# Performance work log

Hardware: AMD Instinct MI355X
Metric: run time of the kernel (lower is better)

Reference implementation:

```python
import math
import jax, jax.numpy as jnp
import numpy as np

B, L, ENC_IN, D_MODEL, D_FF, E_LAYERS, N_HEADS, FACTOR = 4, 2048, 32, 512, 2048, 2, 8, 5


def layer_norm(x, g, b, eps=1e-5):
    mu = jnp.mean(x, axis=-1, keepdims=True)
    var = jnp.mean((x - mu) ** 2, axis=-1, keepdims=True)
    return (x - mu) / jnp.sqrt(var + eps) * g + b


def positional_encoding(length, d_model):
    pos = np.arange(length, dtype=np.float32)[:, None]
    div = np.exp(np.arange(0, d_model, 2, dtype=np.float32) * -(math.log(10000.0) / d_model))
    pe = np.zeros((length, d_model), dtype=np.float32)
    pe[:, 0::2] = np.sin(pos * div)
    pe[:, 1::2] = np.cos(pos * div)
    return jnp.asarray(pe)


def circ_conv1d(x, w, b=None):
    # x: [B,L,Cin], w: [Cout,Cin,3]; kernel 3, circular padding 1, stride 1 -> [B,L,Cout]
    xc = jnp.transpose(x, (0, 2, 1))
    xc = jnp.pad(xc, ((0, 0), (0, 0), (1, 1)), mode='wrap')
    y = jax.lax.conv_general_dilated(xc, w, (1,), 'VALID',
                                     dimension_numbers=('NCH', 'OIH', 'NCH'))
    if b is not None:
        y = y + b[None, :, None]
    return jnp.transpose(y, (0, 2, 1))


def prob_attention(Q, K, V, key):
    # Q,K,V: [B,H,L,D]; ProbAttention(mask_flag=False, factor=5)
    Bq, H, Lq, D = Q.shape
    sample_k = min(FACTOR * int(math.ceil(math.log(Lq))), Lq)  # U_part
    n_top = min(FACTOR * int(math.ceil(math.log(Lq))), Lq)    # u
    idx = jax.random.randint(key, (Lq, sample_k), 0, Lq)
    K_samp = K[:, :, idx, :]                                  # [B,H,L,sample_k,D]
    QK_samp = jnp.einsum('bhld,bhlud->bhlu', Q, K_samp)
    M = QK_samp.max(axis=-1) - QK_samp.sum(axis=-1) / Lq      # sparsity measure [B,H,L]
    _, M_top = jax.lax.top_k(M, n_top)                        # [B,H,u]
    Q_red = jnp.take_along_axis(Q, M_top[..., None], axis=2)  # [B,H,u,D]
    scores = jnp.einsum('bhud,bhkd->bhuk', Q_red, K) / math.sqrt(D)
    attn = jax.nn.softmax(scores, axis=-1)
    upd = jnp.einsum('bhuk,bhkd->bhud', attn, V)
    # initial context = mean of V (mask_flag=False), overwritten at top-u rows
    ctx = jnp.broadcast_to(jnp.mean(V, axis=2, keepdims=True), (Bq, H, Lq, D))
    bi = jnp.arange(Bq)[:, None, None]
    hi = jnp.arange(H)[None, :, None]
    return ctx.at[bi, hi, M_top].set(upd)


def attention_layer(x, Wq, bq, Wk, bk, Wv, bv, Wo, bo, key):
    Bx, Lx, dm = x.shape
    D = dm // N_HEADS
    def split(h):
        return h.reshape(Bx, Lx, N_HEADS, D).transpose(0, 2, 1, 3)
    q = split(x @ Wq.T + bq)
    k = split(x @ Wk.T + bk)
    v = split(x @ Wv.T + bv)
    ctx = prob_attention(q, k, v, key)
    ctx = ctx.transpose(0, 2, 1, 3).reshape(Bx, Lx, dm)
    return ctx @ Wo.T + bo


def encoder_layer(x, Wq, bq, Wk, bk, Wv, bv, Wo, bo, W1, b1, W2, b2, g1, be1, g2, be2, key):
    x = x + attention_layer(x, Wq, bq, Wk, bk, Wv, bv, Wo, bo, key)
    x = layer_norm(x, g1, be1)
    y = jax.nn.gelu(x @ W1.T + b1, approximate=False)  # conv1 (kernel 1) + gelu
    y = y @ W2.T + b2                                  # conv2 (kernel 1)
    return layer_norm(x + y, g2, be2)


def conv_distil(x, w, b, bn_g, bn_b):
    y = circ_conv1d(x, w, b)
    mu = jnp.mean(y, axis=(0, 1))                      # BatchNorm1d (training-mode stats)
    var = jnp.mean((y - mu) ** 2, axis=(0, 1))
    y = (y - mu) / jnp.sqrt(var + 1e-5) * bn_g + bn_b
    y = jax.nn.elu(y)
    yt = jnp.transpose(y, (0, 2, 1))                   # MaxPool1d(k=3, s=2, p=1)
    yt = jax.lax.reduce_window(yt, -jnp.inf, jax.lax.max,
                               (1, 1, 3), (1, 1, 2), [(0, 0), (0, 0), (1, 1)])
    return jnp.transpose(yt, (0, 2, 1))


def setup_inputs() -> dict:
    key = jax.random.key(0)
    ks = iter(jax.random.split(key, 32))
    def nrm(shape, sc=0.02):
        return jax.random.normal(next(ks), shape, jnp.float32) * sc
    return {
        'x_enc': jax.random.normal(next(ks), (B, L, ENC_IN), jnp.float32),
        'tok_w': nrm((D_MODEL, ENC_IN, 3), 0.1),
        'Wq': nrm((E_LAYERS, D_MODEL, D_MODEL)), 'bq': jnp.zeros((E_LAYERS, D_MODEL)),
        'Wk': nrm((E_LAYERS, D_MODEL, D_MODEL)), 'bk': jnp.zeros((E_LAYERS, D_MODEL)),
        'Wv': nrm((E_LAYERS, D_MODEL, D_MODEL)), 'bv': jnp.zeros((E_LAYERS, D_MODEL)),
        'Wo': nrm((E_LAYERS, D_MODEL, D_MODEL)), 'bo': jnp.zeros((E_LAYERS, D_MODEL)),
        'W1': nrm((E_LAYERS, D_FF, D_MODEL)), 'b1': jnp.zeros((E_LAYERS, D_FF)),
        'W2': nrm((E_LAYERS, D_MODEL, D_FF)), 'b2': jnp.zeros((E_LAYERS, D_MODEL)),
        'ln1_g': jnp.ones((E_LAYERS, D_MODEL)), 'ln1_b': jnp.zeros((E_LAYERS, D_MODEL)),
        'ln2_g': jnp.ones((E_LAYERS, D_MODEL)), 'ln2_b': jnp.zeros((E_LAYERS, D_MODEL)),
        'conv_w': nrm((D_MODEL, D_MODEL, 3)), 'conv_b': jnp.zeros((D_MODEL,)),
        'bn_g': jnp.ones((D_MODEL,)), 'bn_b': jnp.zeros((D_MODEL,)),
        'normf_g': jnp.ones((D_MODEL,)), 'normf_b': jnp.zeros((D_MODEL,)),
        'proj_w': nrm((ENC_IN, D_MODEL)), 'proj_b': jnp.zeros((ENC_IN,)),
    }


def reference(x_enc, tok_w, Wq, bq, Wk, bk, Wv, bv, Wo, bo, W1, b1, W2, b2,
              ln1_g, ln1_b, ln2_g, ln2_b, conv_w, conv_b, bn_g, bn_b,
              normf_g, normf_b, proj_w, proj_b):
    keys = jax.random.split(jax.random.key(42), E_LAYERS)
    # DataEmbedding: circular token conv (no bias) + sinusoidal positional embedding
    x = circ_conv1d(x_enc, tok_w) + positional_encoding(x_enc.shape[1], D_MODEL)[None]
    for i in range(E_LAYERS):
        x = encoder_layer(x, Wq[i], bq[i], Wk[i], bk[i], Wv[i], bv[i], Wo[i], bo[i],
                          W1[i], b1[i], W2[i], b2[i],
                          ln1_g[i], ln1_b[i], ln2_g[i], ln2_b[i], keys[i])
        if i == 0:  # single distillation ConvLayer after first encoder layer
            x = conv_distil(x, conv_w, conv_b, bn_g, bn_b)
    x = layer_norm(x, normf_g, normf_b)
    out = x @ proj_w.T + proj_b
    return out[:, :L]  # [:, :seq_len] slice (no-op after distillation halves length)
```

## Files before the change

kernel.cpp:

```cpp
#include <hip/hip_runtime.h>
#include <cstdint>
#include <cmath>


#define NB 4
#define DM 512
#define NH 8
#define HD 64
#define QS 1536

typedef unsigned short ushort_t;
typedef __bf16 bf16x8 __attribute__((ext_vector_type(8)));
typedef float floatx4 __attribute__((ext_vector_type(4)));
typedef unsigned short ushort8_t __attribute__((ext_vector_type(8)));

__device__ inline ushort_t f2b(float f) {
  uint32_t u = __float_as_uint(f);
  uint32_t r = (u + 0x7fffu + ((u >> 16) & 1u)) >> 16;
  return (ushort_t)r;
}
__device__ inline float b2f(ushort_t u) {
  return __uint_as_float((uint32_t)u << 16);
}

__global__ void castqkv_k(const float* __restrict__ Wq,
                          const float* __restrict__ Wk,
                          const float* __restrict__ Wv,
                          ushort_t* __restrict__ out) {
  int gid = blockIdx.x * 256 + threadIdx.x;
  if (gid >= 393216) return;
  int ly = gid / 196608, r4 = gid - ly * 196608;
  int r = r4 >> 7, c4 = r4 & 127;
  int sel = r >> 9, srow = r & 511;
  const float* src = (sel == 0 ? Wq : sel == 1 ? Wk : Wv) + ly * 262144 +
                     srow * 512 + c4 * 4;
  float4 v = *(const float4*)src;
  ushort4 o;
  o.x = f2b(v.x); o.y = f2b(v.y); o.z = f2b(v.z); o.w = f2b(v.w);
  ((ushort4*)out)[ly * 196608 + r * 128 + c4] = o;
}

__global__ void castw3_k(const float* __restrict__ Wo,
                         const float* __restrict__ W1,
                         const float* __restrict__ W2,
                         const float* __restrict__ tw,
                         ushort_t* __restrict__ oWo, ushort_t* __restrict__ oW1,
                         ushort_t* __restrict__ oW2, ushort_t* __restrict__ otw) {
  int gid = blockIdx.x * 256 + threadIdx.x;
  if (gid >= 1191936) return;
  const float* src;
  ushort4* dst;
  int i;
  if (gid < 131072) { src = Wo; dst = (ushort4*)oWo; i = gid; }
  else if (gid < 655360) { src = W1; dst = (ushort4*)oW1; i = gid - 131072; }
  else if (gid < 1179648) { src = W2; dst = (ushort4*)oW2; i = gid - 655360; }
  else { src = tw; dst = (ushort4*)otw; i = gid - 1179648; }
  float4 v = ((const float4*)src)[i];
  ushort4 o;
  o.x = f2b(v.x); o.y = f2b(v.y); o.z = f2b(v.z); o.w = f2b(v.w);
  dst[i] = o;
}

__global__ void castw_conv_k(const float* __restrict__ in,
                             ushort_t* __restrict__ out) {
  int gid = blockIdx.x * 256 + threadIdx.x;
  int d = gid / 1536, r = gid - d * 1536;
  int t = r >> 9, i = r & 511;
  out[gid] = f2b(in[d * 1536 + i * 3 + t]);
}

__global__ void castproj_k(const float* __restrict__ w,
                           float* __restrict__ wt) {
  int gid = blockIdx.x * 256 + threadIdx.x;
  int k = gid >> 5, n = gid & 31;
  wt[gid] = w[n * 512 + k];
}

__global__ void setup_small_k(const float* __restrict__ bq,
                              const float* __restrict__ bk,
                              const float* __restrict__ bv,
                              float* __restrict__ ZB,
                              float* __restrict__ BQKV) {
  int gid = blockIdx.x * 256 + threadIdx.x;
  if (gid >= 3584) return;
  if (gid < 512) { ZB[gid] = 0.f; return; }
  int g = gid - 512;
  int layer = g / 1536, r = g - layer * 1536;
  float v;
  if (r < 512) v = bq[layer * 512 + r];
  else if (r < 1024) v = bk[layer * 512 + r - 512];
  else v = bv[layer * 512 + r - 1024];
  BQKV[g] = v;
}

__host__ __device__ inline void threefry2x32(uint32_t k0, uint32_t k1,
                                             uint32_t c0, uint32_t c1,
                                             uint32_t* o0, uint32_t* o1) {
  uint32_t ks0 = k0, ks1 = k1, ks2 = k0 ^ k1 ^ 0x1BD11BDAu;
  uint32_t x0 = c0 + ks0;
  uint32_t x1 = c1 + ks1;
  const uint32_t rotA[4] = {13u, 15u, 26u, 6u};
  const uint32_t rotB[4] = {17u, 29u, 16u, 24u};
  uint32_t ks[3] = {ks0, ks1, ks2};
  #pragma unroll
  for (int i = 0; i < 5; ++i) {
    const uint32_t* r = (i & 1) ? rotB : rotA;
    #pragma unroll
    for (int j = 0; j < 4; ++j) {
      x0 += x1;
      x1 = (x1 << r[j]) | (x1 >> (32u - r[j]));
      x1 ^= x0;
    }
    x0 += ks[(i + 1) % 3];
    x1 += ks[(i + 2) % 3] + (uint32_t)(i + 1);
  }
  *o0 = x0; *o1 = x1;
}

__global__ void gen_idx_k(int* __restrict__ idx, int n, int mask,
                          uint32_t k0, uint32_t k1) {
  int i = blockIdx.x * 256 + threadIdx.x;
  if (i < n) {
    uint32_t o0, o1;
    threefry2x32(k0, k1, 0u, (uint32_t)i, &o0, &o1);
    idx[i] = (int)((o0 ^ o1) & (uint32_t)mask);
  }
}

__device__ inline float wave_sum64(float v) {
  #pragma unroll
  for (int o = 32; o > 0; o >>= 1) v += __shfl_xor(v, o, 64);
  return v;
}

__global__ void pe_k(float* __restrict__ pe) {
  int i = blockIdx.x * 256 + threadIdx.x;
  int d = i & 511, l = i >> 9;
  int j2 = d & ~1;
  float div = expf((float)j2 * -1.7988946039e-2f);
  float ang = (float)l * div;
  pe[i] = (d & 1) ? cosf(ang) : sinf(ang);
}

__global__ void im2col_tok_k(const float* __restrict__ xe,
                             ushort_t* __restrict__ A) {
  int gid = blockIdx.x * 256 + threadIdx.x;
  int col = gid % 96;
  int row = gid / 96;
  int c = col / 3, t = col - c * 3;
  int b = row >> 11, l = row & 2047;
  int ls = (l + t - 1) & 2047;
  A[gid] = f2b(xe[((size_t)b * 2048 + ls) * 32 + c]);
}

__device__ inline void gload16(const ushort_t* g, ushort_t* l) {
  __builtin_amdgcn_global_load_lds(
      (const __attribute__((address_space(1))) unsigned int*)(const void*)g,
      (__attribute__((address_space(3))) unsigned int*)(void*)l, 16, 0, 0);
}

template <int TM, int CONV, int GELU, int OMODE, int ADDPE, int SPLITK>
__global__ __launch_bounds__(512, 4) void mgemm_k(
    const ushort_t* __restrict__ A, const ushort_t* __restrict__ W,
    const float* __restrict__ bias, float* __restrict__ Cf,
    float* __restrict__ Cf2, ushort_t* __restrict__ Cb,
    const float* __restrict__ pe, int X, int ldc, int K) {
  constexpr int MT = TM / 64;
  constexpr int AG = TM / 128;
  constexpr int BUFSZ = (TM + 128) * 32;
  constexpr int SHSZ = (2 * BUFSZ > 18432) ? 2 * BUFSZ : 18432;
  __shared__ __align__(16) ushort_t SH[SHSZ];
  int id = blockIdx.x;
  int half = 0;
  if (SPLITK == 2) {
    int nb = gridDim.x >> 1;
    if (id >= nb) { half = 1; id -= nb; }
  }
  int kbase = half * (K >> 1);
  int KK = (SPLITK == 2) ? (K >> 1) : K;
  int cc = id & 7, j = id >> 3;
  int bx = j % X;
  int by = (j / X) * 8 + cc;
  int m0 = by * TM, n0 = bx * 128;
  int t = threadIdx.x;
  int lane = t & 63, wv = t >> 6;
  int rl = lane >> 2, cl = (lane & 3) * 8;
  int RaA = wv * (16 * AG);
  int RaB = wv * 16;
  const ushort_t* gA[AG];
  int cbv[AG], clrv[AG], lAoff[AG];
  #pragma unroll
  for (int g = 0; g < AG; ++g) {
    int ar = m0 + RaA + g * 16 + rl;
    gA[g] = A + (size_t)ar * K + kbase + cl;
    cbv[g] = ar >> 11;
    clrv[g] = ar & 2047;
    lAoff[g] = (RaA + g * 16) * 32;
  }
  const ushort_t* gB = W + (size_t)(n0 + RaB + rl) * K + kbase + cl;
  int lBoff = TM * 32 + RaB * 32;

  int quad = lane >> 4, lr = lane & 15;
  int wm = wv >> 1, wn = wv & 1;

  floatx4 acc[MT][4] = {};
  #pragma unroll
  for (int g = 0; g < AG; ++g) {
    if (CONV) {
      int kg = kbase;
      int tt = kg >> 9;
      int c = (kg & 511) + cl;
      int ls = (clrv[g] + tt - 1) & 2047;
      gload16(A + ((size_t)(cbv[g] * 2048 + ls) * 512 + c), SH + lAoff[g]);
    } else {
      gload16(gA[g], SH + lAoff[g]);
    }
  }
  gload16(gB, SH + lBoff);
  __syncthreads();
  int cur = 0;
  for (int ks = 0; ks < KK; ks += 32) {
    int nxt = ks + 32;
    if (nxt < KK) {
      int bb = (cur ^ 1) * BUFSZ;
      #pragma unroll
      for (int g = 0; g < AG; ++g) {
        if (CONV) {
          int kg = kbase + nxt;
          int tt = kg >> 9;
          int c = (kg & 511) + cl;
          int ls = (clrv[g] + tt - 1) & 2047;
          gload16(A + ((size_t)(cbv[g] * 2048 + ls) * 512 + c),
                  SH + bb + lAoff[g]);
        } else {
          gload16(gA[g] + nxt, SH + bb + lAoff[g]);
        }
      }
      gload16(gB + nxt, SH + bb + lBoff);
    }
    const ushort_t* Ab = SH + cur * BUFSZ;
    const ushort_t* Bb = Ab + TM * 32;
    bf16x8 av[MT], bv[4];
    #pragma unroll
    for (int mt = 0; mt < MT; ++mt)
      av[mt] =
          *(const bf16x8*)&Ab[(wm * (16 * MT) + mt * 16 + lr) * 32 + quad * 8];
    #pragma unroll
    for (int nt = 0; nt < 4; ++nt)
      bv[nt] = *(const bf16x8*)&Bb[(wn * 64 + nt * 16 + lr) * 32 + quad * 8];
    #pragma unroll
    for (int mt = 0; mt < MT; ++mt)
      #pragma unroll
      for (int nt = 0; nt < 4; ++nt)
        acc[mt][nt] = __builtin_amdgcn_mfma_f32_16x16x32_bf16(
            av[mt], bv[nt], acc[mt][nt], 0, 0, 0);
    __syncthreads();
    cur ^= 1;
  }

  if (SPLITK == 2) {
    float* dst = half ? Cf2 : Cf;
    #pragma unroll
    for (int nt = 0; nt < 4; ++nt) {
      int col = n0 + wn * 64 + nt * 16 + lr;
      #pragma unroll
      for (int mt = 0; mt < MT; ++mt) {
        int row0 = m0 + wm * (16 * MT) + mt * 16 + quad * 4;
        #pragma unroll
        for (int r = 0; r < 4; ++r)
          dst[(size_t)(row0 + r) * ldc + col] = acc[mt][nt][r];
      }
    }
  } else if (OMODE == 0) {
    #pragma unroll
    for (int nt = 0; nt < 4; ++nt) {
      int col = n0 + wn * 64 + nt * 16 + lr;
      float bsv = bias[col];
      #pragma unroll
      for (int mt = 0; mt < MT; ++mt) {
        int row0 = m0 + wm * (16 * MT) + mt * 16 + quad * 4;
        #pragma unroll
        for (int r = 0; r < 4; ++r) {
          int row = row0 + r;
          float v = acc[mt][nt][r] + bsv;
          if (ADDPE) v += pe[(size_t)(row & 2047) * ldc + col];
          if (GELU) v = 0.5f * v * (1.0f + erff(v * 0.70710678118654752f));
          Cf[(size_t)row * ldc + col] = v;
        }
      }
    }
  } else {
    ushort_t* ep = SH + wv * 2304;
    #pragma unroll
    for (int p = 0; p < MT / 2; ++p) {
      #pragma unroll
      for (int nt = 0; nt < 4; ++nt) {
        int col = n0 + wn * 64 + nt * 16 + lr;
        float bsv = bias[col];
        #pragma unroll
        for (int ml = 0; ml < 2; ++ml) {
          int mt = p * 2 + ml;
          #pragma unroll
          for (int r = 0; r < 4; ++r) {
            int row = m0 + wm * (16 * MT) + mt * 16 + quad * 4 + r;
            float v = acc[mt][nt][r] + bsv;
            if (ADDPE) v += pe[(size_t)(row & 2047) * ldc + col];
            if (GELU) v = 0.5f * v * (1.0f + erff(v * 0.70710678118654752f));
            if (OMODE == 2) Cf[(size_t)row * ldc + col] = v;
            ep[(ml * 16 + quad * 4 + r) * 72 + nt * 16 + lr] = f2b(v);
          }
        }
      }
      int r8 = lane >> 3, c8 = (lane & 7) * 8;
      #pragma unroll
      for (int i = 0; i < 4; ++i) {
        int row = i * 8 + r8;
        ushort8_t vv = *(const ushort8_t*)&ep[row * 72 + c8];
        *(ushort8_t*)&Cb[(size_t)(m0 + wm * (16 * MT) + p * 32 + row) * ldc +
                         n0 + wn * 64 + c8] = vv;
      }
    }
  }
}

__global__ __launch_bounds__(256) void proj_k(
    const float* __restrict__ A, const float* __restrict__ Wt,
    const float* __restrict__ bias, float* __restrict__ C) {
  int t = threadIdx.x;
  int n = t & 31, ml = t >> 5;
  int m = blockIdx.x * 8 + ml;
  const float* a = A + (size_t)m * DM;
  float a0 = 0.f, a1 = 0.f, a2 = 0.f, a3 = 0.f;
  #pragma unroll 4
  for (int k = 0; k < DM; k += 4) {
    float4 av = *(const float4*)&a[k];
    a0 += av.x * Wt[k * 32 + n];
    a1 += av.y * Wt[(k + 1) * 32 + n];
    a2 += av.z * Wt[(k + 2) * 32 + n];
    a3 += av.w * Wt[(k + 3) * 32 + n];
  }
  C[(size_t)m * 32 + n] = (a0 + a2) + (a1 + a3) + bias[n];
}

__global__ __launch_bounds__(128) void ln_k(
    const float* __restrict__ A, const float* __restrict__ Bres,
    const float* __restrict__ Bres2, const float* __restrict__ cbias,
    const float* __restrict__ g, const float* __restrict__ be,
    float* __restrict__ O, ushort_t* __restrict__ Ob) {
  int r = blockIdx.x, t = threadIdx.x;
  __shared__ float lds[2];
  float4 v = ((const float4*)(A + (size_t)r * DM))[t];
  if (Bres) {
    float4 u = ((const float4*)(Bres + (size_t)r * DM))[t];
    v.x += u.x; v.y += u.y; v.z += u.z; v.w += u.w;
  }
  if (Bres2) {
    float4 u = ((const float4*)(Bres2 + (size_t)r * DM))[t];
    v.x += u.x; v.y += u.y; v.z += u.z; v.w += u.w;
  }
  if (cbias) {
    float4 u = ((const float4*)cbias)[t];
    v.x += u.x; v.y += u.y; v.z += u.z; v.w += u.w;
  }
  float s = wave_sum64(v.x + v.y + v.z + v.w);
  int w = t >> 6;
  if ((t & 63) == 0) lds[w] = s;
  __syncthreads();
  float mu = (lds[0] + lds[1]) * (1.0f / 512.0f);
  __syncthreads();
  float dx = v.x - mu, dy = v.y - mu, dz = v.z - mu, dw = v.w - mu;
  float sq = wave_sum64(dx * dx + dy * dy + dz * dz + dw * dw);
  if ((t & 63) == 0) lds[w] = sq;
  __syncthreads();
  float var = (lds[0] + lds[1]) * (1.0f / 512.0f);
  float inv = 1.0f / sqrtf(var + 1e-5f);
  float4 gv = ((const float4*)g)[t];
  float4 bv = ((const float4*)be)[t];
  float4 o;
  o.x = dx * inv * gv.x + bv.x;
  o.y = dy * inv * gv.y + bv.y;
  o.z = dz * inv * gv.z + bv.z;
  o.w = dw * inv * gv.w + bv.w;
  ((float4*)(O + (size_t)r * DM))[t] = o;
  if (Ob) {
    ushort4 ob;
    ob.x = f2b(o.x); ob.y = f2b(o.y); ob.z = f2b(o.z); ob.w = f2b(o.w);
    ((ushort4*)(Ob + (size_t)r * DM))[t] = ob;
  }
}

template <int UU>
__global__ __launch_bounds__(256) void qk_m_k(
    const ushort_t* __restrict__ QKVb, const int* __restrict__ idx,
    float* __restrict__ Mout, int Lx) {
  int l = blockIdx.x;
  int b = threadIdx.x >> 6;
  int lane = threadIdx.x & 63;
  const ushort_t* qp = QKVb + ((size_t)b * Lx + l) * QS + lane * 8;
  float q[8];
  {
    ushort8_t qv = *(const ushort8_t*)qp;
    #pragma unroll
    for (int c = 0; c < 8; ++c) q[c] = b2f(qv[c]);
  }
  const ushort_t* Kbase = QKVb + (size_t)b * Lx * QS + 512 + lane * 8;
  const int* ip = idx + (size_t)l * UU;
  float maxv = -INFINITY, sumv = 0.f;
  #pragma unroll
  for (int u0 = 0; u0 < UU; u0 += 8) {
    ushort8_t kv[8];
    #pragma unroll
    for (int j = 0; j < 8; ++j) {
      if (u0 + j < UU)
        kv[j] = *(const ushort8_t*)(Kbase + (size_t)ip[u0 + j] * QS);
    }
    #pragma unroll
    for (int j = 0; j < 8; ++j) {
      if (u0 + j < UU) {
        float p = 0.f;
        #pragma unroll
        for (int c = 0; c < 8; ++c) p += q[c] * b2f(kv[j][c]);
        p += __shfl_xor(p, 1, 64);
        p += __shfl_xor(p, 2, 64);
        p += __shfl_xor(p, 4, 64);
        maxv = fmaxf(maxv, p);
        sumv += p;
      }
    }
  }
  if ((lane & 7) == 0) {
    int h = lane >> 3;
    Mout[(size_t)(b * 8 + h) * Lx + l] = maxv - sumv / (float)Lx;
  }
}

__global__ __launch_bounds__(1024) void topk_k(
    const float* __restrict__ Mbuf, int* __restrict__ Mtop, int Lx, int U) {
  int nch = Lx >> 8;
  int bh = blockIdx.x / nch, ch = blockIdx.x % nch;
  const float* m = Mbuf + (size_t)bh * Lx;
  __shared__ float sm[2048];
  __shared__ int part[1024];
  int t = threadIdx.x;
  int c = t & 255, q = t >> 8;
  for (int i = t; i < Lx; i += 1024) sm[i] = m[i];
  __syncthreads();
  int i0 = (ch << 8) + c;
  float v0 = sm[i0];
  int r0 = 0;
  int qlen = Lx >> 2;
  int j0 = q * qlen, j1 = j0 + qlen;
  for (int j = j0; j < j1; j += 4) {
    float4 mj = *(const float4*)&sm[j];
    r0 += (mj.x > v0) || (mj.x == v0 && (j + 0) < i0);
    r0 += (mj.y > v0) || (mj.y == v0 && (j + 1) < i0);
    r0 += (mj.z > v0) || (mj.z == v0 && (j + 2) < i0);
    r0 += (mj.w > v0) || (mj.w == v0 && (j + 3) < i0);
  }
  part[t] = r0;
  __syncthreads();
  if (q == 0) {
    int r = part[c] + part[c + 256] + part[c + 512] + part[c + 768];
    if (r < U) Mtop[bh * U + r] = i0;
  }
}

__global__ __launch_bounds__(512) void meanv1_k(const ushort_t* __restrict__ QKVb,
                                                float* __restrict__ part,
                                                int Lx) {
  int b = blockIdx.x >> 4, chunk = blockIdx.x & 15;
  int rows = Lx >> 4;
  int t = threadIdx.x;
  const ushort_t* vp =
      QKVb + ((size_t)b * Lx + (size_t)chunk * rows) * QS + 1024 + t;
  float s = 0.f;
  for (int l = 0; l < rows; ++l) s += b2f(vp[(size_t)l * QS]);
  part[(size_t)blockIdx.x * DM + t] = s;
}
__global__ __launch_bounds__(512) void meanv2_k(const float* __restrict__ part,
                                                float* __restrict__ mv,
                                                int Lx) {
  int b = blockIdx.x, t = threadIdx.x;
  float s = 0.f;
  #pragma unroll
  for (int c = 0; c < 16; ++c) s += part[(size_t)(b * 16 + c) * DM + t];
  mv[b * DM + t] = s / (float)Lx;
}

__global__ void fillctx_k(ushort_t* __restrict__ ctx,
                          const float* __restrict__ mv, int Lx) {
  size_t i4 = (size_t)blockIdx.x * 256 + threadIdx.x;
  int col4 = (int)(i4 & 127);
  size_t row = i4 >> 7;
  int b = (int)(row / (size_t)Lx);
  const float* m = mv + b * DM + col4 * 4;
  ushort4 o;
  o.x = f2b(m[0]); o.y = f2b(m[1]); o.z = f2b(m[2]); o.w = f2b(m[3]);
  ((ushort4*)ctx)[i4] = o;
}

template <int UP>
__global__ __launch_bounds__(256) void attn_mfma_k(
    const ushort_t* __restrict__ QKVb, const int* __restrict__ Mtop,
    float* __restrict__ part, int Lx, int U, int nblk) {
  __shared__ ushort_t Ps[4][UP * 72];
  __shared__ ushort_t Vs[4][64 * 64];
  int bh = blockIdx.x / nblk, blkc = blockIdx.x % nblk;
  int h = bh & 7, b = bh >> 3;
  int t = threadIdx.x;
  int wv = t >> 6, lane = t & 63;
  int quad = lane >> 4, lr = lane & 15;
  int chunk = blkc * 4 + wv;
  int k0 = chunk * 64;
  const ushort_t* Qb = QKVb + (size_t)b * Lx * QS + h * HD;
  const ushort_t* Kb = Qb + 512;
  const ushort_t* Vb = Qb + 1024;

  bf16x8 qf[3][2];
  #pragma unroll
  for (int mt = 0; mt < 3; ++mt) {
    int u = mt * 16 + lr;
    int qi = Mtop[bh * U + (u < U ? u : U - 1)];
    const ushort_t* qp = Qb + (size_t)qi * QS + quad * 8;
    qf[mt][0] = *(const bf16x8*)qp;
    qf[mt][1] = *(const bf16x8*)(qp + 32);
  }

  ushort_t* vs = Vs[wv];
  #pragma unroll
  for (int i = 0; i < 8; ++i) {
    int cid = i * 64 + lane;
    int k = cid >> 3, c = cid & 7;
    ushort8_t v = *(const ushort8_t*)(Vb + (size_t)(k0 + k) * QS + c * 8);
    *(ushort8_t*)&vs[k * 64 + ((c * 8) ^ (((k >> 3) & 3) << 4))] = v;
  }

  floatx4 Sa[3][4] = {};
  #pragma unroll
  for (int kt = 0; kt < 4; ++kt) {
    const ushort_t* kp = Kb + (size_t)(k0 + kt * 16 + lr) * QS + quad * 8;
    bf16x8 kf0 = *(const bf16x8*)kp;
    bf16x8 kf1 = *(const bf16x8*)(kp + 32);
    #pragma unroll
    for (int mt = 0; mt < 3; ++mt) {
      Sa[mt][kt] = __builtin_amdgcn_mfma_f32_16x16x32_bf16(
          qf[mt][0], kf0, Sa[mt][kt], 0, 0, 0);
      Sa[mt][kt] = __builtin_amdgcn_mfma_f32_16x16x32_bf16(
          qf[mt][1], kf1, Sa[mt][kt], 0, 0, 0);
    }
  }

  float m_[3][4], l_[3][4];
  #pragma unroll
  for (int mt = 0; mt < 3; ++mt) {
    #pragma unroll
    for (int kt = 0; kt < 4; ++kt) Sa[mt][kt] *= 0.125f;
    #pragma unroll
    for (int r = 0; r < 4; ++r) {
      float mx = fmaxf(fmaxf(Sa[mt][0][r], Sa[mt][1][r]),
                       fmaxf(Sa[mt][2][r], Sa[mt][3][r]));
      #pragma unroll
      for (int o = 1; o <= 8; o <<= 1) mx = fmaxf(mx, __shfl_xor(mx, o, 64));
      float rs = 0.f;
      #pragma unroll
      for (int kt = 0; kt < 4; ++kt) {
        float e = __expf(Sa[mt][kt][r] - mx);
        Sa[mt][kt][r] = e;
        rs += e;
      }
      #pragma unroll
      for (int o = 1; o <= 8; o <<= 1) rs += __shfl_xor(rs, o, 64);
      m_[mt][r] = mx;
      l_[mt][r] = rs;
    }
  }

  ushort_t* ps = Ps[wv];
  floatx4 Oa[3][4] = {};
  #pragma unroll
  for (int pass = 0; pass < 2; ++pass) {
    #pragma unroll
    for (int mt = 0; mt < 3; ++mt)
      #pragma unroll
      for (int kt = 0; kt < 4; ++kt)
        #pragma unroll
        for (int r = 0; r < 4; ++r) {
          float e = Sa[mt][kt][r];
          ushort_t hb = f2b(e);
          ps[(mt * 16 + quad * 4 + r) * 72 + kt * 16 + lr] = hb;
          Sa[mt][kt][r] = e - b2f(hb);
        }
    #pragma unroll
    for (int kk = 0; kk < 2; ++kk) {
      bf16x8 pf[3];
      #pragma unroll
      for (int mt = 0; mt < 3; ++mt)
        pf[mt] = *(const bf16x8*)&ps[(mt * 16 + lr) * 72 + kk * 32 + quad * 8];
      #pragma unroll
      for (int nt = 0; nt < 4; ++nt) {
        ushort8_t vt;
        #pragma unroll
        for (int j = 0; j < 8; ++j)
          vt[j] = vs[(kk * 32 + quad * 8 + j) * 64 +
                     ((nt * 16 + lr) ^ (quad << 4))];
        bf16x8 vf = *(bf16x8*)&vt;
        #pragma unroll
        for (int mt = 0; mt < 3; ++mt)
          Oa[mt][nt] = __builtin_amdgcn_mfma_f32_16x16x32_bf16(
              pf[mt], vf, Oa[mt][nt], 0, 0, 0);
      }
    }
  }

  float* pb = part + (size_t)(bh * (nblk * 4) + chunk) * U * 66;
  #pragma unroll
  for (int mt = 0; mt < 3; ++mt) {
    #pragma unroll
    for (int r = 0; r < 4; ++r) {
      int u = mt * 16 + quad * 4 + r;
      if (u < U) {
        #pragma unroll
        for (int nt = 0; nt < 4; ++nt)
          pb[(size_t)u * 66 + nt * 16 + lr] = Oa[mt][nt][r];
        if (lr == 0) {
          pb[(size_t)u * 66 + 64] = m_[mt][r];
          pb[(size_t)u * 66 + 65] = l_[mt][r];
        }
      }
    }
  }
}

__global__ __launch_bounds__(64) void attn_merge_k(
    const float* __restrict__ part, const int* __restrict__ Mtop,
    ushort_t* __restrict__ ctx, int Lx, int U, int nchunk) {
  int bu = blockIdx.x;
  int u = bu % U, bh = bu / U;
  int h = bh & 7, b = bh >> 3;
  int d = threadIdx.x;
  float M = -INFINITY;
  for (int c = 0; c < nchunk; ++c)
    M = fmaxf(M, part[((size_t)(bh * nchunk + c) * U + u) * 66 + 64]);
  float L = 0.f, O = 0.f;
  for (int c = 0; c < nchunk; ++c) {
    const float* pp = part + ((size_t)(bh * nchunk + c) * U + u) * 66;
    float w = __expf(pp[64] - M);
    L += pp[65] * w;
    O += pp[d] * w;
  }
  int qi = Mtop[bh * U + u];
  ctx[((size_t)b * Lx + qi) * DM + h * HD + d] = f2b(O / L);
}

__global__ __launch_bounds__(256) void bn1_k(const float* __restrict__ Y0,
                                             const float* __restrict__ Y1,
                                             const float* __restrict__ cb,
                                             float* __restrict__ ps,
                                             float* __restrict__ pq) {
  int blk = blockIdx.x;
  int t = threadIdx.x;
  float cb0 = cb[t], cb1 = cb[t + 256];
  float s0 = 0, q0 = 0, s1 = 0, q1 = 0;
  const float* b0 = Y0 + (size_t)blk * 256 * DM;
  const float* b1 = Y1 + (size_t)blk * 256 * DM;
  for (int r = 0; r < 256; ++r) {
    float a = b0[(size_t)r * DM + t] + b1[(size_t)r * DM + t] + cb0;
    float b = b0[(size_t)r * DM + t + 256] + b1[(size_t)r * DM + t + 256] + cb1;
    s0 += a; q0 += a * a; s1 += b; q1 += b * b;
  }
  ps[blk * DM + t] = s0; ps[blk * DM + t + 256] = s1;
  pq[blk * DM + t] = q0; pq[blk * DM + t + 256] = q1;
}
__global__ __launch_bounds__(512) void bn2_k(const float* __restrict__ ps,
                                             const float* __restrict__ pq,
                                             float* __restrict__ mu,
                                             float* __restrict__ var) {
  int t = threadIdx.x;
  float s = 0, q = 0;
  #pragma unroll
  for (int c = 0; c < 32; ++c) { s += ps[c * DM + t]; q += pq[c * DM + t]; }
  float m = s * (1.0f / 8192.f);
  mu[t] = m;
  var[t] = q * (1.0f / 8192.f) - m * m;
}

__global__ void bnpool_k(const float* __restrict__ Y0,
                         const float* __restrict__ Y1,
                         const float* __restrict__ cb,
                         const float* __restrict__ mu,
                         const float* __restrict__ var,
                         const float* __restrict__ g,
                         const float* __restrict__ be, float* __restrict__ O,
                         ushort_t* __restrict__ Ob) {
  size_t i = (size_t)blockIdx.x * 256 + threadIdx.x;
  int c = (int)(i & 511);
  size_t row = i >> 9;
  int lo = (int)(row & 1023);
  int b = (int)(row >> 10);
  float sc = g[c] / sqrtf(var[c] + 1e-5f);
  float sh = be[c] - mu[c] * sc;
  float cbv = cb[c];
  int l0 = 2 * lo - 1;
  float m = -INFINITY;
  #pragma unroll
  for (int tt = 0; tt < 3; ++tt) {
    int l = l0 + tt;
    if (l >= 0 && l < 2048) {
      size_t off = ((size_t)b * 2048 + l) * DM + c;
      float v = (Y0[off] + Y1[off] + cbv) * sc + sh;
      v = v > 0.f ? v : expm1f(v);
      m = fmaxf(m, v);
    }
  }
  O[i] = m;
  Ob[i] = f2b(m);
}

extern "C" void kernel_launch(void* const* d_in, const int* in_sizes, int n_in,
                              void* d_out, int out_size, void* d_ws,
                              size_t ws_size, hipStream_t stream) {
  (void)in_sizes; (void)n_in; (void)out_size; (void)ws_size;
  const float* x_enc  = (const float*)d_in[0];
  const float* tok_w  = (const float*)d_in[1];
  const float* Wq     = (const float*)d_in[2];
  const float* bq     = (const float*)d_in[3];
  const float* Wk     = (const float*)d_in[4];
  const float* bk     = (const float*)d_in[5];
  const float* Wv     = (const float*)d_in[6];
  const float* bv     = (const float*)d_in[7];
  const float* Wo     = (const float*)d_in[8];
  const float* bo     = (const float*)d_in[9];
  const float* W1     = (const float*)d_in[10];
  const float* b1     = (const float*)d_in[11];
  const float* W2     = (const float*)d_in[12];
  const float* b2     = (const float*)d_in[13];
  const float* ln1_g  = (const float*)d_in[14];
  const float* ln1_b  = (const float*)d_in[15];
  const float* ln2_g  = (const float*)d_in[16];
  const float* ln2_b  = (const float*)d_in[17];
  const float* conv_w = (const float*)d_in[18];
  const float* conv_b = (const float*)d_in[19];
  const float* bn_g   = (const float*)d_in[20];
  const float* bn_b   = (const float*)d_in[21];
  const float* normf_g = (const float*)d_in[22];
  const float* normf_b = (const float*)d_in[23];
  const float* proj_w = (const float*)d_in[24];
  const float* proj_b = (const float*)d_in[25];
  float* out = (float*)d_out;
  float* ws = (float*)d_ws;

  float* X    = ws;
  float* Y2B  = ws + 4194304;
  float* SCR  = ws + 8388608;
  ushort_t* CTXb = (ushort_t*)(ws + 16777216);
  float* Y2   = ws + 20971520;
  float* Mb   = ws + 25165824;
  float* MV   = ws + 25231360;
  float* MVP  = ws + 25233408;
  float* BNps = ws + 25266176;
  float* BNpq = ws + 25282560;
  float* BNmu = ws + 25298944;
  float* BNvr = ws + 25299456;
  float* ZB   = ws + 25299968;
  float* BQKV = ws + 25300480;
  int*   IDX  = (int*)(ws + 25303552);
  int*   MT   = (int*)(ws + 25385472);
  ushort_t* U0   = (ushort_t*)(ws + 25386752);
  ushort_t* Xb   = U0;
  ushort_t* Hb   = U0 + 4194304;
  ushort_t* QKVb = Hb;
  ushort_t* Wqkvb= U0 + 20971520;
  ushort_t* Wob  = U0 + 22544384;
  ushort_t* W1b  = U0 + 23068672;
  ushort_t* W2b  = U0 + 25165824;
  ushort_t* Cwb  = U0 + 27262976;
  ushort_t* Twb  = U0 + 28049408;
  ushort_t* Atok = U0 + 28098560;
  float* PEf = ws + 39829248;
  float* PWt = ws + 40877824;

  castqkv_k<<<1536, 256, 0, stream>>>(Wq, Wk, Wv, Wqkvb);
  castw3_k<<<4656, 256, 0, stream>>>(Wo, W1, W2, tok_w, Wob, W1b, W2b, Twb);
  castw_conv_k<<<3072, 256, 0, stream>>>(conv_w, Cwb);
  castproj_k<<<64, 256, 0, stream>>>(proj_w, PWt);
  setup_small_k<<<14, 256, 0, stream>>>(bq, bk, bv, ZB, BQKV);
  pe_k<<<4096, 256, 0, stream>>>(PEf);
  im2col_tok_k<<<3072, 256, 0, stream>>>(x_enc, Atok);

  mgemm_k<128, 0, 0, 2, 1, 1><<<256, 512, 0, stream>>>(
      Atok, Twb, ZB, X, nullptr, Xb, PEf, 4, DM, 96);

  for (int layer = 0; layer < 2; ++layer) {
    const int Lx = (layer == 0) ? 2048 : 1024;
    const int U  = (layer == 0) ? 40 : 35;
    const int M  = NB * Lx;
    const int Yt = M / 128;
    const int NCHT = Lx / 64;
    const int NBLK = NCHT / 4;

    uint32_t kl0, kl1, s0, s1;
    threefry2x32(0u, 42u, 0u, (uint32_t)layer, &kl0, &kl1);
    threefry2x32(kl0, kl1, 0u, 1u, &s0, &s1);
    int nidx = Lx * U;
    gen_idx_k<<<(nidx + 255) / 256, 256, 0, stream>>>(IDX, nidx, Lx - 1, s0, s1);

    mgemm_k<128, 0, 0, 1, 0, 1><<<12 * Yt, 512, 0, stream>>>(
        Xb, Wqkvb + (size_t)layer * 786432, BQKV + layer * 1536, nullptr,
        nullptr, QKVb, nullptr, 12, QS, DM);

    if (layer == 0)
      qk_m_k<40><<<Lx, 256, 0, stream>>>(QKVb, IDX, Mb, Lx);
    else
      qk_m_k<35><<<Lx, 256, 0, stream>>>(QKVb, IDX, Mb, Lx);
    topk_k<<<NB * NH * (Lx >> 8), 1024, 0, stream>>>(Mb, MT, Lx, U);
    meanv1_k<<<NB * 16, 512, 0, stream>>>(QKVb, MVP, Lx);
    meanv2_k<<<NB, 512, 0, stream>>>(MVP, MV, Lx);
    fillctx_k<<<(M * DM / 4) / 256, 256, 0, stream>>>(CTXb, MV, Lx);
    attn_mfma_k<48><<<NB * NH * NBLK, 256, 0, stream>>>(QKVb, MT, Y2, Lx, U,
                                                        NBLK);
    attn_merge_k<<<NB * NH * U, 64, 0, stream>>>(Y2, MT, CTXb, Lx, U, NCHT);

    mgemm_k<128, 0, 0, 0, 0, 2><<<2 * 4 * Yt, 512, 0, stream>>>(
        CTXb, Wob + (size_t)layer * 262144, nullptr, Y2, Y2B, nullptr,
        nullptr, 4, DM, DM);
    ln_k<<<M, 128, 0, stream>>>(X, Y2, Y2B, bo + layer * DM,
                                ln1_g + layer * DM, ln1_b + layer * DM, X, Xb);

    mgemm_k<128, 0, 1, 1, 0, 1><<<16 * Yt, 512, 0, stream>>>(
        Xb, W1b + (size_t)layer * 1048576, b1 + layer * 2048, nullptr, nullptr,
        Hb, nullptr, 16, 2048, DM);
    mgemm_k<128, 0, 0, 0, 0, 2><<<2 * 4 * Yt, 512, 0, stream>>>(
        Hb, W2b + (size_t)layer * 1048576, nullptr, Y2, Y2B, nullptr,
        nullptr, 4, DM, 2048);
    ln_k<<<M, 128, 0, stream>>>(X, Y2, Y2B, b2 + layer * DM,
                                ln2_g + layer * DM, ln2_b + layer * DM, X, Xb);

    if (layer == 0) {
      mgemm_k<128, 1, 0, 0, 0, 2><<<2 * 4 * 64, 512, 0, stream>>>(
          Xb, Cwb, nullptr, Y2, Y2B, nullptr, nullptr, 4, DM, 1536);
      bn1_k<<<32, 256, 0, stream>>>(Y2, Y2B, conv_b, BNps, BNpq);
      bn2_k<<<1, 512, 0, stream>>>(BNps, BNpq, BNmu, BNvr);
      bnpool_k<<<(NB * 1024 * 512) / 256, 256, 0, stream>>>(
          Y2, Y2B, conv_b, BNmu, BNvr, bn_g, bn_b, X, Xb);
    }
  }

  ln_k<<<NB * 1024, 128, 0, stream>>>(X, nullptr, nullptr, nullptr, normf_g,
                                      normf_b, SCR, nullptr);
  proj_k<<<512, 256, 0, stream>>>(SCR, PWt, proj_b, out);
}
```

Measured before the change: 618.3 us.

## Triple-buffer GEMM LDS pipeline with explicit vmcnt waits and single barrier

```diff
diff --git a/kernel.cpp b/kernel.cpp
--- a/kernel.cpp
+++ b/kernel.cpp
@@ -168,7 +168,7 @@
   constexpr int MT = TM / 64;
   constexpr int AG = TM / 128;
   constexpr int BUFSZ = (TM + 128) * 32;
-  constexpr int SHSZ = (2 * BUFSZ > 18432) ? 2 * BUFSZ : 18432;
+  constexpr int SHSZ = (3 * BUFSZ > 18432) ? 3 * BUFSZ : 18432;
   __shared__ __align__(16) ushort_t SH[SHSZ];
   int id = blockIdx.x;
   int half = 0;
@@ -203,40 +203,46 @@
   int quad = lane >> 4, lr = lane & 15;
   int wm = wv >> 1, wn = wv & 1;
 
+  auto STAGE = [&](int kst, int buf) {
+    int bb = buf * BUFSZ;
+    int ko = kst << 5;
+    #pragma unroll
+    for (int g = 0; g < AG; ++g) {
+      if (CONV) {
+        int kg = kbase + ko;
+        int tt = kg >> 9;
+        int c = (kg & 511) + cl;
+        int ls = (clrv[g] + tt - 1) & 2047;
+        gload16(A + ((size_t)(cbv[g] * 2048 + ls) * 512 + c),
+                SH + bb + lAoff[g]);
+      } else {
+        gload16(gA[g] + ko, SH + bb + lAoff[g]);
+      }
+    }
+    gload16(gB + ko, SH + bb + lBoff);
+  };
+
   floatx4 acc[MT][4] = {};
-  #pragma unroll
-  for (int g = 0; g < AG; ++g) {
-    if (CONV) {
-      int kg = kbase;
-      int tt = kg >> 9;
-      int c = (kg & 511) + cl;
-      int ls = (clrv[g] + tt - 1) & 2047;
-      gload16(A + ((size_t)(cbv[g] * 2048 + ls) * 512 + c), SH + lAoff[g]);
+  int nt = KK >> 5;
+  STAGE(0, 0);
+  if (nt > 1) STAGE(1, 1);
+  int cur = 0;
+  for (int it = 0; it < nt; ++it) {
+    if (it < nt - 1) {
+      if constexpr (AG == 1)
+        asm volatile("s_waitcnt vmcnt(2)" ::: "memory");
+      else
+        asm volatile("s_waitcnt vmcnt(3)" ::: "memory");
     } else {
-      gload16(gA[g], SH + lAoff[g]);
-    }
-  }
-  gload16(gB, SH + lBoff);
-  __syncthreads();
-  int cur = 0;
-  for (int ks = 0; ks < KK; ks += 32) {
-    int nxt = ks + 32;
-    if (nxt < KK) {
-      int bb = (cur ^ 1) * BUFSZ;
-      #pragma unroll
-      for (int g = 0; g < AG; ++g) {
-        if (CONV) {
-          int kg = kbase + nxt;
-          int tt = kg >> 9;
-          int c = (kg & 511) + cl;
-          int ls = (clrv[g] + tt - 1) & 2047;
-          gload16(A + ((size_t)(cbv[g] * 2048 + ls) * 512 + c),
-                  SH + bb + lAoff[g]);
-        } else {
-          gload16(gA[g] + nxt, SH + bb + lAoff[g]);
-        }
-      }
-      gload16(gB + nxt, SH + bb + lBoff);
+      asm volatile("s_waitcnt vmcnt(0)" ::: "memory");
+    }
+    __builtin_amdgcn_s_barrier();
+    __builtin_amdgcn_sched_barrier(0);
+    int nx = it + 2;
+    if (nx < nt) {
+      int nb3 = cur + 2;
+      if (nb3 >= 3) nb3 -= 3;
+      STAGE(nx, nb3);
     }
     const ushort_t* Ab = SH + cur * BUFSZ;
     const ushort_t* Bb = Ab + TM * 32;
@@ -246,35 +252,37 @@
       av[mt] =
           *(const bf16x8*)&Ab[(wm * (16 * MT) + mt * 16 + lr) * 32 + quad * 8];
     #pragma unroll
-    for (int nt = 0; nt < 4; ++nt)
-      bv[nt] = *(const bf16x8*)&Bb[(wn * 64 + nt * 16 + lr) * 32 + quad * 8];
+    for (int nt2 = 0; nt2 < 4; ++nt2)
+      bv[nt2] = *(const bf16x8*)&Bb[(wn * 64 + nt2 * 16 + lr) * 32 + quad * 8];
     #pragma unroll
     for (int mt = 0; mt < MT; ++mt)
       #pragma unroll
-      for (int nt = 0; nt < 4; ++nt)
-        acc[mt][nt] = __builtin_amdgcn_mfma_f32_16x16x32_bf16(
-            av[mt], bv[nt], acc[mt][nt], 0, 0, 0);
-    __syncthreads();
-    cur ^= 1;
-  }
+      for (int nt2 = 0; nt2 < 4; ++nt2)
+        acc[mt][nt2] = __builtin_amdgcn_mfma_f32_16x16x32_bf16(
+            av[mt], bv[nt2], acc[mt][nt2], 0, 0, 0);
+    asm volatile("s_waitcnt lgkmcnt(0)" ::: "memory");
+    __builtin_amdgcn_sched_barrier(0);
+    cur = (cur == 2) ? 0 : cur + 1;
+  }
+  __syncthreads();
 
   if (SPLITK == 2) {
     float* dst = half ? Cf2 : Cf;
     #pragma unroll
-    for (int nt = 0; nt < 4; ++nt) {
-      int col = n0 + wn * 64 + nt * 16 + lr;
+    for (int nt2 = 0; nt2 < 4; ++nt2) {
+      int col = n0 + wn * 64 + nt2 * 16 + lr;
       #pragma unroll
       for (int mt = 0; mt < MT; ++mt) {
         int row0 = m0 + wm * (16 * MT) + mt * 16 + quad * 4;
         #pragma unroll
         for (int r = 0; r < 4; ++r)
-          dst[(size_t)(row0 + r) * ldc + col] = acc[mt][nt][r];
+          dst[(size_t)(row0 + r) * ldc + col] = acc[mt][nt2][r];
       }
     }
   } else if (OMODE == 0) {
     #pragma unroll
-    for (int nt = 0; nt < 4; ++nt) {
-      int col = n0 + wn * 64 + nt * 16 + lr;
+    for (int nt2 = 0; nt2 < 4; ++nt2) {
+      int col = n0 + wn * 64 + nt2 * 16 + lr;
       float bsv = bias[col];
       #pragma unroll
       for (int mt = 0; mt < MT; ++mt) {
@@ -282,7 +290,7 @@
         #pragma unroll
         for (int r = 0; r < 4; ++r) {
           int row = row0 + r;
-          float v = acc[mt][nt][r] + bsv;
+          float v = acc[mt][nt2][r] + bsv;
           if (ADDPE) v += pe[(size_t)(row & 2047) * ldc + col];
           if (GELU) v = 0.5f * v * (1.0f + erff(v * 0.70710678118654752f));
           Cf[(size_t)row * ldc + col] = v;
@@ -294,8 +302,8 @@
     #pragma unroll
     for (int p = 0; p < MT / 2; ++p) {
       #pragma unroll
-      for (int nt = 0; nt < 4; ++nt) {
-        int col = n0 + wn * 64 + nt * 16 + lr;
+      for (int nt2 = 0; nt2 < 4; ++nt2) {
+        int col = n0 + wn * 64 + nt2 * 16 + lr;
         float bsv = bias[col];
         #pragma unroll
         for (int ml = 0; ml < 2; ++ml) {
@@ -303,11 +311,11 @@
           #pragma unroll
           for (int r = 0; r < 4; ++r) {
             int row = m0 + wm * (16 * MT) + mt * 16 + quad * 4 + r;
-            float v = acc[mt][nt][r] + bsv;
+            float v = acc[mt][nt2][r] + bsv;
             if (ADDPE) v += pe[(size_t)(row & 2047) * ldc + col];
             if (GELU) v = 0.5f * v * (1.0f + erff(v * 0.70710678118654752f));
             if (OMODE == 2) Cf[(size_t)row * ldc + col] = v;
-            ep[(ml * 16 + quad * 4 + r) * 72 + nt * 16 + lr] = f2b(v);
+            ep[(ml * 16 + quad * 4 + r) * 72 + nt2 * 16 + lr] = f2b(v);
           }
         }
       }
```

Result: faster. 601.1 us (-2.8%).
